# Performance work log

Hardware: AMD Instinct MI355X
Metric: run time of the kernel (lower is better)

The kernel has to match this reference:

```python
import jax, jax.numpy as jnp
import numpy as np

N_NODES = 100000
N_EDGES = 1600000
N_FEAT = 128
N_HID = 128


def cheb_conv_k2(x, edge_index, W0, W1, b):
    """PyG ChebConv with K=2, sym norm, lambda_max=2.0.
    Reduces to: out = x @ W0 + (L_hat x) @ W1 + b, where
    L_hat = 2L/lambda_max - I = -D^{-1/2} A D^{-1/2} (diagonal cancels).
    """
    n = x.shape[0]
    row, col = edge_index[0], edge_index[1]
    deg = jax.ops.segment_sum(jnp.ones_like(row, dtype=x.dtype), row, num_segments=n)
    dinv = jnp.where(deg > 0, jax.lax.rsqrt(jnp.maximum(deg, 1.0)), 0.0)
    w = -(dinv[row] * dinv[col])                     # [E] edge weights of L_hat
    tx1 = jax.ops.segment_sum(x[col] * w[:, None], row, num_segments=n)  # [N, F]
    return x @ W0 + tx1 @ W1 + b


def setup_inputs() -> dict:
    key = jax.random.key(0)
    ks = jax.random.split(key, 8)
    glorot = lambda k, fi, fo: jax.random.normal(k, (fi, fo), dtype=jnp.float32) * np.float32(np.sqrt(2.0 / (fi + fo)))
    x = jax.random.normal(ks[0], (N_NODES, N_FEAT), dtype=jnp.float32)
    edge_index = jax.random.randint(ks[1], (2, N_EDGES), 0, N_NODES, dtype=jnp.int64 if jax.config.jax_enable_x64 else jnp.int32)
    return {
        "x": x,
        "edge_index": edge_index,
        "W0_1": glorot(ks[2], N_FEAT, N_HID),
        "W1_1": glorot(ks[3], N_FEAT, N_HID),
        "b1": jnp.zeros((N_HID,), dtype=jnp.float32),
        "W0_2": glorot(ks[4], N_HID, N_HID),
        "W1_2": glorot(ks[5], N_HID, N_HID),
        "b2": jnp.zeros((N_HID,), dtype=jnp.float32),
    }


def reference(x, edge_index, W0_1, W1_1, b1, W0_2, W1_2, b2):
    # eval mode: input Dropout, dropout_adj(p=0.8), and per-layer Dropout are identity
    x1 = jax.nn.relu(cheb_conv_k2(x, edge_index, W0_1, W1_1, b1))
    x2 = jax.nn.relu(cheb_conv_k2(x1, edge_index, W0_2, W1_2, b2))
    # mean of the two layer outputs; outAct is identity
    return (x1 + x2) * 0.5
```

## Files before the change

### kernel.cpp

```cpp
#include <hip/hip_runtime.h>

#define NN 100000
#define NE 1600000
#define NF 128
#define NSTRIP (NN / 16)
#define NBUCK ((NN + 127) / 128)
#define CAP 2560
#define CHUNK 4096

typedef __attribute__((ext_vector_type(8))) short short8;
typedef __attribute__((ext_vector_type(4))) float f32x4;

__device__ __forceinline__ unsigned short f2b(float f) {
    union { float f; unsigned int u; } v; v.f = f;
    unsigned int u = v.u;
    unsigned int r = (u + 0x7fffu + ((u >> 16) & 1u)) >> 16;
    return (unsigned short)r;
}

__global__ __launch_bounds__(256) void k_init(int* __restrict__ gcur) {
    int i = blockIdx.x * 256 + threadIdx.x;
    if (i < NBUCK) gcur[i] = i * CAP;
}

__global__ __launch_bounds__(256) void k_bin(const int* __restrict__ row,
                                             const int* __restrict__ col,
                                             int* __restrict__ gcur,
                                             unsigned int* __restrict__ gslab) {
    __shared__ int hist[NBUCK];
    __shared__ int start[NBUCK];
    __shared__ int gbase[NBUCK];
    __shared__ int scanbuf[256];
    __shared__ unsigned int stage[CHUNK];
    __shared__ unsigned short sb[CHUNK];

    const int t = threadIdx.x;
    const int e0 = blockIdx.x * CHUNK;
    const int cnt = min(CHUNK, NE - e0);

    for (int i = t; i < NBUCK; i += 256) hist[i] = 0;
    __syncthreads();
    for (int i = t; i < cnt; i += 256) atomicAdd(&hist[row[e0 + i] >> 7], 1);
    __syncthreads();

    const int b0 = t * 4;
    int s = 0;
#pragma unroll
    for (int k = 0; k < 4; ++k) { int idx = b0 + k; if (idx < NBUCK) s += hist[idx]; }
    scanbuf[t] = s;
    __syncthreads();
    for (int off = 1; off < 256; off <<= 1) {
        int u = t >= off ? scanbuf[t - off] : 0;
        __syncthreads();
        scanbuf[t] += u;
        __syncthreads();
    }
    int run = t > 0 ? scanbuf[t - 1] : 0;
#pragma unroll
    for (int k = 0; k < 4; ++k) {
        int idx = b0 + k;
        if (idx < NBUCK) { start[idx] = run; run += hist[idx]; }
    }
    __syncthreads();

    for (int i = t; i < NBUCK; i += 256) {
        int c = hist[i];
        gbase[i] = c > 0 ? atomicAdd(&gcur[i], c) : 0;
        hist[i] = start[i];
    }
    __syncthreads();

    for (int i = t; i < cnt; i += 256) {
        int r = row[e0 + i];
        int b = r >> 7;
        int p = atomicAdd(&hist[b], 1);
        stage[p] = (unsigned int)col[e0 + i] | ((unsigned int)(r & 127) << 17);
        sb[p] = (unsigned short)b;
    }
    __syncthreads();

    for (int i = t; i < cnt; i += 256) {
        int b = sb[i];
        gslab[gbase[b] + (i - start[b])] = stage[i];
    }
}

__global__ __launch_bounds__(256) void k_bscan(const int* __restrict__ gcur,
                                               int* __restrict__ bbase) {
    __shared__ int s[NBUCK];
    int t = threadIdx.x;
    for (int i = t; i < NBUCK; i += 256) s[i] = gcur[i] - i * CAP;
    __syncthreads();
    if (t == 0) {
        int run = 0;
        for (int i = 0; i < NBUCK; ++i) { int v = s[i]; s[i] = run; run += v; }
    }
    __syncthreads();
    for (int i = t; i < NBUCK; i += 256) bbase[i] = s[i];
}

__global__ __launch_bounds__(256) void k_csr(const unsigned int* __restrict__ gslab,
                                             const int* __restrict__ gcur,
                                             const int* __restrict__ bbase,
                                             int* __restrict__ offs,
                                             int* __restrict__ ccol,
                                             float* __restrict__ dinv) {
    __shared__ int rh[128];
    __shared__ int rcur[128];
    __shared__ unsigned int scol[CAP];

    const int b = blockIdx.x;
    const int segbase = b * CAP;
    const int cnt = gcur[b] - segbase;
    const int csr0 = bbase[b];
    const int t = threadIdx.x;

    if (t < 128) rh[t] = 0;
    __syncthreads();
    for (int i = t; i < cnt; i += 256) atomicAdd(&rh[gslab[segbase + i] >> 17], 1);
    __syncthreads();
    if (t == 0) {
        int run = 0;
        for (int r = 0; r < 128; ++r) { rcur[r] = run; run += rh[r]; }
    }
    __syncthreads();

    const int rbase = b * 128;
    if (t < 128 && rbase + t < NN) {
        offs[rbase + t] = csr0 + rcur[t];
        int d = rh[t];
        dinv[rbase + t] = d > 0 ? rsqrtf((float)d) : 0.0f;
    }
    if (b == NBUCK - 1 && t == 0) offs[NN] = NE;
    __syncthreads();

    for (int i = t; i < cnt; i += 256) {
        unsigned int v = gslab[segbase + i];
        int p = atomicAdd(&rcur[v >> 17], 1);
        scol[p] = v & 0x1ffff;
    }
    __syncthreads();
    for (int i = t; i < cnt; i += 256) ccol[csr0 + i] = scol[i];
}

__global__ __launch_bounds__(256) void k_quant(const float* __restrict__ x,
                                               const float* __restrict__ dinv,
                                               unsigned short* __restrict__ xq,
                                               float* __restrict__ dsc,
                                               float* __restrict__ sx) {
    int r = (blockIdx.x * 256 + threadIdx.x) >> 6;
    int lane = threadIdx.x & 63;
    float2 v = ((const float2*)x)[r * 64 + lane];
    float m = fmaxf(fabsf(v.x), fabsf(v.y));
#pragma unroll
    for (int mask = 32; mask; mask >>= 1) m = fmaxf(m, __shfl_xor(m, mask));
    float s = m * (1.0f / 127.0f);
    float inv = m > 0.0f ? 127.0f / m : 0.0f;
    int qx = (int)rintf(v.x * inv) + 128;
    int qy = (int)rintf(v.y * inv) + 128;
    xq[r * 64 + lane] = (unsigned short)(qx | (qy << 8));
    if (lane == 0) { dsc[r] = dinv[r] * s; sx[r] = s; }
}

__global__ __launch_bounds__(256) void k_pack(const float* __restrict__ W01,
                                              const float* __restrict__ W11,
                                              const float* __restrict__ W02,
                                              const float* __restrict__ W12,
                                              unsigned short* __restrict__ WP) {
    int idx = blockIdx.x * 256 + threadIdx.x;
    int mi = idx >> 14;
    int e = idx & 16383;
    const float* W = mi == 0 ? W01 : mi == 1 ? W02 : mi == 2 ? W11 : W12;
    int midx = mi == 0 ? 0 : mi == 1 ? 2 : mi == 2 ? 1 : 3;
    int k = e >> 7, n = e & 127;
    int kt = k >> 5, g = (k >> 3) & 3, j = k & 7;
    WP[midx * 16384 + (((kt * 4 + g) * 128 + n) << 3) + j] = f2b(W[e]);
}

__global__ __launch_bounds__(256) void k_gather(const int* __restrict__ offs,
                                                const int* __restrict__ ccol,
                                                const float* __restrict__ dsc,
                                                const float* __restrict__ dinv,
                                                const uint2* __restrict__ xq64,
                                                uint4* __restrict__ txb4,
                                                float qbias) {
    int r = (blockIdx.x * 256 + threadIdx.x) >> 6;
    if (r >= NN) return;
    int lane = threadIdx.x & 63;
    int fl = lane & 15, q = lane >> 4;
    int beg = offs[r], end = offs[r + 1];
    float a0 = 0.f, a1 = 0.f, a2 = 0.f, a3 = 0.f;
    float a4 = 0.f, a5 = 0.f, a6 = 0.f, a7 = 0.f, S = 0.f;
    int j = beg + q;
    for (; j + 12 < end; j += 16) {
        int c0 = ccol[j], c1 = ccol[j + 4], c2 = ccol[j + 8], c3 = ccol[j + 12];
        float w0 = dsc[c0], w1 = dsc[c1], w2 = dsc[c2], w3 = dsc[c3];
        uint2 u0 = xq64[c0 * 16 + fl];
        uint2 u1 = xq64[c1 * 16 + fl];
        uint2 u2 = xq64[c2 * 16 + fl];
        uint2 u3 = xq64[c3 * 16 + fl];
        a0 += w0 * (float)(u0.x & 0xffu)         + w1 * (float)(u1.x & 0xffu)
            + w2 * (float)(u2.x & 0xffu)         + w3 * (float)(u3.x & 0xffu);
        a1 += w0 * (float)((u0.x >> 8) & 0xffu)  + w1 * (float)((u1.x >> 8) & 0xffu)
            + w2 * (float)((u2.x >> 8) & 0xffu)  + w3 * (float)((u3.x >> 8) & 0xffu);
        a2 += w0 * (float)((u0.x >> 16) & 0xffu) + w1 * (float)((u1.x >> 16) & 0xffu)
            + w2 * (float)((u2.x >> 16) & 0xffu) + w3 * (float)((u3.x >> 16) & 0xffu);
        a3 += w0 * (float)(u0.x >> 24)           + w1 * (float)(u1.x >> 24)
            + w2 * (float)(u2.x >> 24)           + w3 * (float)(u3.x >> 24);
        a4 += w0 * (float)(u0.y & 0xffu)         + w1 * (float)(u1.y & 0xffu)
            + w2 * (float)(u2.y & 0xffu)         + w3 * (float)(u3.y & 0xffu);
        a5 += w0 * (float)((u0.y >> 8) & 0xffu)  + w1 * (float)((u1.y >> 8) & 0xffu)
            + w2 * (float)((u2.y >> 8) & 0xffu)  + w3 * (float)((u3.y >> 8) & 0xffu);
        a6 += w0 * (float)((u0.y >> 16) & 0xffu) + w1 * (float)((u1.y >> 16) & 0xffu)
            + w2 * (float)((u2.y >> 16) & 0xffu) + w3 * (float)((u3.y >> 16) & 0xffu);
        a7 += w0 * (float)(u0.y >> 24)           + w1 * (float)(u1.y >> 24)
            + w2 * (float)(u2.y >> 24)           + w3 * (float)(u3.y >> 24);
        S += w0 + w1 + w2 + w3;
    }
    for (; j < end; j += 4) {
        int c = ccol[j];
        float w = dsc[c];
        uint2 u = xq64[c * 16 + fl];
        a0 += w * (float)(u.x & 0xffu);
        a1 += w * (float)((u.x >> 8) & 0xffu);
        a2 += w * (float)((u.x >> 16) & 0xffu);
        a3 += w * (float)(u.x >> 24);
        a4 += w * (float)(u.y & 0xffu);
        a5 += w * (float)((u.y >> 8) & 0xffu);
        a6 += w * (float)((u.y >> 16) & 0xffu);
        a7 += w * (float)(u.y >> 24);
        S += w;
    }
#pragma unroll
    for (int mask = 32; mask >= 16; mask >>= 1) {
        a0 += __shfl_xor(a0, mask); a1 += __shfl_xor(a1, mask);
        a2 += __shfl_xor(a2, mask); a3 += __shfl_xor(a3, mask);
        a4 += __shfl_xor(a4, mask); a5 += __shfl_xor(a5, mask);
        a6 += __shfl_xor(a6, mask); a7 += __shfl_xor(a7, mask);
        S  += __shfl_xor(S, mask);
    }
    if (q == 0) {
        float s = -dinv[r];
        float qb = qbias * S;
        a0 = s * (a0 - qb); a1 = s * (a1 - qb); a2 = s * (a2 - qb); a3 = s * (a3 - qb);
        a4 = s * (a4 - qb); a5 = s * (a5 - qb); a6 = s * (a6 - qb); a7 = s * (a7 - qb);
        uint4 o;
        o.x = (unsigned int)f2b(a0) | ((unsigned int)f2b(a1) << 16);
        o.y = (unsigned int)f2b(a2) | ((unsigned int)f2b(a3) << 16);
        o.z = (unsigned int)f2b(a4) | ((unsigned int)f2b(a5) << 16);
        o.w = (unsigned int)f2b(a6) | ((unsigned int)f2b(a7) << 16);
        txb4[r * 16 + fl] = o;
    }
}

__global__ __launch_bounds__(256) void k_mm(const unsigned char* __restrict__ Aq,
                                            const float* __restrict__ s_in,
                                            float qoff,
                                            const unsigned short* __restrict__ Tbf,
                                            const unsigned short* __restrict__ WP0,
                                            const unsigned short* __restrict__ WP1,
                                            const float* __restrict__ bias,
                                            const float* __restrict__ dinv,
                                            float* __restrict__ out,
                                            unsigned char* __restrict__ Qout,
                                            float* __restrict__ dsc_out,
                                            float* __restrict__ s1_out,
                                            int mode) {
    int wid = (blockIdx.x * 256 + threadIdx.x) >> 6;
    if (wid >= NSTRIP) return;
    int lane = threadIdx.x & 63;
    int g = lane >> 4, m = lane & 15;

    short8 a[4], t[4];
    {
        float sA = s_in[wid * 16 + m];
        const unsigned char* Arow = Aq + (size_t)(wid * 16 + m) * NF + g * 8;
#pragma unroll
        for (int kt = 0; kt < 4; ++kt) {
            uint2 u = *(const uint2*)(Arow + kt * 32);
            short8 v;
            v[0] = f2b(sA * ((float)(u.x & 0xffu) - qoff));
            v[1] = f2b(sA * ((float)((u.x >> 8) & 0xffu) - qoff));
            v[2] = f2b(sA * ((float)((u.x >> 16) & 0xffu) - qoff));
            v[3] = f2b(sA * ((float)(u.x >> 24) - qoff));
            v[4] = f2b(sA * ((float)(u.y & 0xffu) - qoff));
            v[5] = f2b(sA * ((float)((u.y >> 8) & 0xffu) - qoff));
            v[6] = f2b(sA * ((float)((u.y >> 16) & 0xffu) - qoff));
            v[7] = f2b(sA * ((float)(u.y >> 24) - qoff));
            a[kt] = v;
        }
    }

    const short8* Tfr = (const short8*)(Tbf + (size_t)(wid * 16 + m) * NF + g * 8);
#pragma unroll
    for (int kt = 0; kt < 4; ++kt) t[kt] = Tfr[kt * 4];

    const short8* B0 = (const short8*)WP0 + g * 128 + m;
    const short8* B1 = (const short8*)WP1 + g * 128 + m;

    f32x4 acc[8];
#pragma unroll
    for (int nt = 0; nt < 8; ++nt) {
        float b = bias[nt * 16 + m];
        acc[nt][0] = b; acc[nt][1] = b; acc[nt][2] = b; acc[nt][3] = b;
    }

#pragma unroll
    for (int nt = 0; nt < 8; ++nt) {
#pragma unroll
        for (int kt = 0; kt < 4; ++kt) {
            acc[nt] = __builtin_amdgcn_mfma_f32_16x16x32_bf16(a[kt], B0[kt * 512 + nt * 16], acc[nt], 0, 0, 0);
            acc[nt] = __builtin_amdgcn_mfma_f32_16x16x32_bf16(t[kt], B1[kt * 512 + nt * 16], acc[nt], 0, 0, 0);
        }
    }

#pragma unroll
    for (int nt = 0; nt < 8; ++nt)
#pragma unroll
        for (int r = 0; r < 4; ++r) acc[nt][r] = fmaxf(acc[nt][r], 0.0f);

    int rbase = wid * 16 + g * 4;
    if (mode == 0) {
        float mr[4] = {0.0f, 0.0f, 0.0f, 0.0f};
#pragma unroll
        for (int nt = 0; nt < 8; ++nt)
#pragma unroll
            for (int r = 0; r < 4; ++r) mr[r] = fmaxf(mr[r], acc[nt][r]);
#pragma unroll
        for (int mask = 1; mask < 16; mask <<= 1)
#pragma unroll
            for (int r = 0; r < 4; ++r) mr[r] = fmaxf(mr[r], __shfl_xor(mr[r], mask));

        float inv[4], s1v[4];
#pragma unroll
        for (int r = 0; r < 4; ++r) {
            s1v[r] = mr[r] * (1.0f / 255.0f);
            inv[r] = mr[r] > 0.0f ? 255.0f / mr[r] : 0.0f;
        }
#pragma unroll
        for (int nt = 0; nt < 8; ++nt) {
            int c = nt * 16 + m;
#pragma unroll
            for (int r = 0; r < 4; ++r) {
                int q = (int)rintf(acc[nt][r] * inv[r]);
                q = q > 255 ? 255 : q;
                Qout[(size_t)(rbase + r) * NF + c] = (unsigned char)q;
            }
        }
        if (m == 0) {
#pragma unroll
            for (int r = 0; r < 4; ++r) {
                s1_out[rbase + r] = s1v[r];
                dsc_out[rbase + r] = dinv[rbase + r] * s1v[r];
            }
        }
    } else {
        float sR[4];
#pragma unroll
        for (int r = 0; r < 4; ++r) sR[r] = s_in[rbase + r];
#pragma unroll
        for (int nt = 0; nt < 8; ++nt) {
            int c = nt * 16 + m;
#pragma unroll
            for (int r = 0; r < 4; ++r) {
                size_t o = (size_t)(rbase + r) * NF + c;
                float x1v = sR[r] * (float)Aq[o];
                out[o] = 0.5f * (x1v + acc[nt][r]);
            }
        }
    }
}

extern "C" void kernel_launch(void* const* d_in, const int* in_sizes, int n_in,
                              void* d_out, int out_size, void* d_ws, size_t ws_size,
                              hipStream_t stream) {
    const float* x   = (const float*)d_in[0];
    const int*   ei  = (const int*)d_in[1];
    const float* W01 = (const float*)d_in[2];
    const float* W11 = (const float*)d_in[3];
    const float* b1  = (const float*)d_in[4];
    const float* W02 = (const float*)d_in[5];
    const float* W12 = (const float*)d_in[6];
    const float* b2  = (const float*)d_in[7];
    float* out = (float*)d_out;

    const int* row = ei;
    const int* col = ei + NE;

    char* ws = (char*)d_ws;
    int*            gcur  = (int*)(ws);
    int*            bbase = (int*)(ws + 3200);
    float*          dinv  = (float*)(ws + 6400);
    int*            offs  = (int*)(ws + 406400);
    int*            ccol  = (int*)(ws + 806416);
    unsigned short* WP    = (unsigned short*)(ws + 7206416);
    float*          dsc   = (float*)(ws + 7337488);
    float*          s1a   = (float*)(ws + 7737488);
    float*          sx    = (float*)(ws + 8137488);
    unsigned short* xq    = (unsigned short*)(ws + 8537488);
    unsigned int*   txb   = (unsigned int*)(ws + 21337488);
    unsigned int*   gslab = (unsigned int*)(ws + 21337488);

    unsigned char*  xq8 = (unsigned char*)xq;
    unsigned short* WP01 = WP;
    unsigned short* WP11 = WP + 16384;
    unsigned short* WP02 = WP + 32768;
    unsigned short* WP12 = WP + 49152;

    k_init <<<(NBUCK + 255) / 256, 256, 0, stream>>>(gcur);
    k_bin  <<<(NE + CHUNK - 1) / CHUNK, 256, 0, stream>>>(row, col, gcur, gslab);
    k_bscan<<<1, 256, 0, stream>>>(gcur, bbase);
    k_csr  <<<NBUCK, 256, 0, stream>>>(gslab, gcur, bbase, offs, ccol, dinv);

    k_quant<<<(NN * 64) / 256, 256, 0, stream>>>(x, dinv, xq, dsc, sx);
    k_pack <<<(4 * 16384) / 256, 256, 0, stream>>>(W01, W11, W02, W12, WP);

    const int gatherBlocks = (NN * 64) / 256;
    const int mmBlocks = (NSTRIP * 64 + 255) / 256;

    k_gather<<<gatherBlocks, 256, 0, stream>>>(offs, ccol, dsc, dinv,
                                               (const uint2*)xq, (uint4*)txb, 128.0f);
    k_mm    <<<mmBlocks, 256, 0, stream>>>(xq8, sx, 128.0f, (const unsigned short*)txb,
                                           WP01, WP11, b1, dinv, out, xq8, dsc, s1a, 0);

    k_gather<<<gatherBlocks, 256, 0, stream>>>(offs, ccol, dsc, dinv,
                                               (const uint2*)xq, (uint4*)txb, 0.0f);
    k_mm    <<<mmBlocks, 256, 0, stream>>>(xq8, s1a, 0.0f, (const unsigned short*)txb,
                                           WP02, WP12, b2, dinv, out, xq8, dsc, s1a, 1);
}
```

Measured before the change: 245.0 us.

## Quantize aggregated features to int8, double rows per wave in matmul, fold init kernel

```diff
diff --git a/kernel.cpp b/kernel.cpp
--- a/kernel.cpp
+++ b/kernel.cpp
@@ -3,7 +3,7 @@
 #define NN 100000
 #define NE 1600000
 #define NF 128
-#define NSTRIP (NN / 16)
+#define NSTRIP2 (NN / 32)
 #define NBUCK ((NN + 127) / 128)
 #define CAP 2560
 #define CHUNK 4096
@@ -16,11 +16,6 @@
     unsigned int u = v.u;
     unsigned int r = (u + 0x7fffu + ((u >> 16) & 1u)) >> 16;
     return (unsigned short)r;
-}
-
-__global__ __launch_bounds__(256) void k_init(int* __restrict__ gcur) {
-    int i = blockIdx.x * 256 + threadIdx.x;
-    if (i < NBUCK) gcur[i] = i * CAP;
 }
 
 __global__ __launch_bounds__(256) void k_bin(const int* __restrict__ row,
@@ -166,8 +161,10 @@
                                               const float* __restrict__ W11,
                                               const float* __restrict__ W02,
                                               const float* __restrict__ W12,
-                                              unsigned short* __restrict__ WP) {
+                                              unsigned short* __restrict__ WP,
+                                              int* __restrict__ gcur) {
     int idx = blockIdx.x * 256 + threadIdx.x;
+    if (idx < NBUCK) gcur[idx] = idx * CAP;
     int mi = idx >> 14;
     int e = idx & 16383;
     const float* W = mi == 0 ? W01 : mi == 1 ? W02 : mi == 2 ? W11 : W12;
@@ -182,7 +179,8 @@
                                                 const float* __restrict__ dsc,
                                                 const float* __restrict__ dinv,
                                                 const uint2* __restrict__ xq64,
-                                                uint4* __restrict__ txb4,
+                                                uint2* __restrict__ txq8,
+                                                float* __restrict__ st_out,
                                                 float qbias) {
     int r = (blockIdx.x * 256 + threadIdx.x) >> 6;
     if (r >= NN) return;
@@ -244,19 +242,29 @@
         float qb = qbias * S;
         a0 = s * (a0 - qb); a1 = s * (a1 - qb); a2 = s * (a2 - qb); a3 = s * (a3 - qb);
         a4 = s * (a4 - qb); a5 = s * (a5 - qb); a6 = s * (a6 - qb); a7 = s * (a7 - qb);
-        uint4 o;
-        o.x = (unsigned int)f2b(a0) | ((unsigned int)f2b(a1) << 16);
-        o.y = (unsigned int)f2b(a2) | ((unsigned int)f2b(a3) << 16);
-        o.z = (unsigned int)f2b(a4) | ((unsigned int)f2b(a5) << 16);
-        o.w = (unsigned int)f2b(a6) | ((unsigned int)f2b(a7) << 16);
-        txb4[r * 16 + fl] = o;
+        float mx = fmaxf(fmaxf(fmaxf(fabsf(a0), fabsf(a1)), fmaxf(fabsf(a2), fabsf(a3))),
+                         fmaxf(fmaxf(fabsf(a4), fabsf(a5)), fmaxf(fabsf(a6), fabsf(a7))));
+#pragma unroll
+        for (int mask = 8; mask; mask >>= 1) mx = fmaxf(mx, __shfl_xor(mx, mask));
+        float st = mx * (1.0f / 127.0f);
+        float invt = mx > 0.0f ? 127.0f / mx : 0.0f;
+        int q0 = (int)rintf(a0 * invt) + 128, q1 = (int)rintf(a1 * invt) + 128;
+        int q2 = (int)rintf(a2 * invt) + 128, q3 = (int)rintf(a3 * invt) + 128;
+        int q4 = (int)rintf(a4 * invt) + 128, q5 = (int)rintf(a5 * invt) + 128;
+        int q6 = (int)rintf(a6 * invt) + 128, q7 = (int)rintf(a7 * invt) + 128;
+        uint2 o;
+        o.x = (unsigned)q0 | ((unsigned)q1 << 8) | ((unsigned)q2 << 16) | ((unsigned)q3 << 24);
+        o.y = (unsigned)q4 | ((unsigned)q5 << 8) | ((unsigned)q6 << 16) | ((unsigned)q7 << 24);
+        txq8[r * 16 + fl] = o;
+        if (fl == 0) st_out[r] = st;
     }
 }
 
 __global__ __launch_bounds__(256) void k_mm(const unsigned char* __restrict__ Aq,
                                             const float* __restrict__ s_in,
                                             float qoff,
-                                            const unsigned short* __restrict__ Tbf,
+                                            const unsigned char* __restrict__ Tq8,
+                                            const float* __restrict__ st_in,
                                             const unsigned short* __restrict__ WP0,
                                             const unsigned short* __restrict__ WP1,
                                             const float* __restrict__ bias,
@@ -267,14 +275,18 @@
                                             float* __restrict__ s1_out,
                                             int mode) {
     int wid = (blockIdx.x * 256 + threadIdx.x) >> 6;
-    if (wid >= NSTRIP) return;
+    if (wid >= NSTRIP2) return;
     int lane = threadIdx.x & 63;
     int g = lane >> 4, m = lane & 15;
 
-    short8 a[4], t[4];
-    {
-        float sA = s_in[wid * 16 + m];
-        const unsigned char* Arow = Aq + (size_t)(wid * 16 + m) * NF + g * 8;
+    short8 a[2][4], t[2][4];
+#pragma unroll
+    for (int s = 0; s < 2; ++s) {
+        int row = wid * 32 + s * 16 + m;
+        float sA = s_in[row];
+        float sT = st_in[row];
+        const unsigned char* Arow = Aq + (size_t)row * NF + g * 8;
+        const unsigned char* Trow = Tq8 + (size_t)row * NF + g * 8;
 #pragma unroll
         for (int kt = 0; kt < 4; ++kt) {
             uint2 u = *(const uint2*)(Arow + kt * 32);
@@ -287,85 +299,109 @@
             v[5] = f2b(sA * ((float)((u.y >> 8) & 0xffu) - qoff));
             v[6] = f2b(sA * ((float)((u.y >> 16) & 0xffu) - qoff));
             v[7] = f2b(sA * ((float)(u.y >> 24) - qoff));
-            a[kt] = v;
+            a[s][kt] = v;
+            uint2 w = *(const uint2*)(Trow + kt * 32);
+            short8 tv;
+            tv[0] = f2b(sT * ((float)(w.x & 0xffu) - 128.0f));
+            tv[1] = f2b(sT * ((float)((w.x >> 8) & 0xffu) - 128.0f));
+            tv[2] = f2b(sT * ((float)((w.x >> 16) & 0xffu) - 128.0f));
+            tv[3] = f2b(sT * ((float)(w.x >> 24) - 128.0f));
+            tv[4] = f2b(sT * ((float)(w.y & 0xffu) - 128.0f));
+            tv[5] = f2b(sT * ((float)((w.y >> 8) & 0xffu) - 128.0f));
+            tv[6] = f2b(sT * ((float)((w.y >> 16) & 0xffu) - 128.0f));
+            tv[7] = f2b(sT * ((float)(w.y >> 24) - 128.0f));
+            t[s][kt] = tv;
         }
     }
-
-    const short8* Tfr = (const short8*)(Tbf + (size_t)(wid * 16 + m) * NF + g * 8);
-#pragma unroll
-    for (int kt = 0; kt < 4; ++kt) t[kt] = Tfr[kt * 4];
 
     const short8* B0 = (const short8*)WP0 + g * 128 + m;
     const short8* B1 = (const short8*)WP1 + g * 128 + m;
 
-    f32x4 acc[8];
+    f32x4 acc[2][8];
 #pragma unroll
     for (int nt = 0; nt < 8; ++nt) {
         float b = bias[nt * 16 + m];
-        acc[nt][0] = b; acc[nt][1] = b; acc[nt][2] = b; acc[nt][3] = b;
+#pragma unroll
+        for (int s = 0; s < 2; ++s) {
+            acc[s][nt][0] = b; acc[s][nt][1] = b; acc[s][nt][2] = b; acc[s][nt][3] = b;
+        }
     }
 
 #pragma unroll
     for (int nt = 0; nt < 8; ++nt) {
 #pragma unroll
         for (int kt = 0; kt < 4; ++kt) {
-            acc[nt] = __builtin_amdgcn_mfma_f32_16x16x32_bf16(a[kt], B0[kt * 512 + nt * 16], acc[nt], 0, 0, 0);
-            acc[nt] = __builtin_amdgcn_mfma_f32_16x16x32_bf16(t[kt], B1[kt * 512 + nt * 16], acc[nt], 0, 0, 0);
-        }
-    }
-
-#pragma unroll
-    for (int nt = 0; nt < 8; ++nt)
-#pragma unroll
-        for (int r = 0; r < 4; ++r) acc[nt][r] = fmaxf(acc[nt][r], 0.0f);
-
-    int rbase = wid * 16 + g * 4;
-    if (mode == 0) {
-        float mr[4] = {0.0f, 0.0f, 0.0f, 0.0f};
-#pragma unroll
-        for (int nt = 0; nt < 8; ++nt)
-#pragma unroll
-            for (int r = 0; r < 4; ++r) mr[r] = fmaxf(mr[r], acc[nt][r]);
-#pragma unroll
-        for (int mask = 1; mask < 16; mask <<= 1)
-#pragma unroll
-            for (int r = 0; r < 4; ++r) mr[r] = fmaxf(mr[r], __shfl_xor(mr[r], mask));
-
-        float inv[4], s1v[4];
-#pragma unroll
-        for (int r = 0; r < 4; ++r) {
-            s1v[r] = mr[r] * (1.0f / 255.0f);
-            inv[r] = mr[r] > 0.0f ? 255.0f / mr[r] : 0.0f;
-        }
-#pragma unroll
-        for (int nt = 0; nt < 8; ++nt) {
-            int c = nt * 16 + m;
-#pragma unroll
-            for (int r = 0; r < 4; ++r) {
-                int q = (int)rintf(acc[nt][r] * inv[r]);
-                q = q > 255 ? 255 : q;
-                Qout[(size_t)(rbase + r) * NF + c] = (unsigned char)q;
+            short8 b0 = B0[kt * 512 + nt * 16];
+            short8 b1 = B1[kt * 512 + nt * 16];
+#pragma unroll
+            for (int s = 0; s < 2; ++s) {
+                acc[s][nt] = __builtin_amdgcn_mfma_f32_16x16x32_bf16(a[s][kt], b0, acc[s][nt], 0, 0, 0);
+                acc[s][nt] = __builtin_amdgcn_mfma_f32_16x16x32_bf16(t[s][kt], b1, acc[s][nt], 0, 0, 0);
             }
         }
-        if (m == 0) {
+    }
+
+#pragma unroll
+    for (int s = 0; s < 2; ++s)
+#pragma unroll
+        for (int nt = 0; nt < 8; ++nt)
+#pragma unroll
+            for (int r = 0; r < 4; ++r) acc[s][nt][r] = fmaxf(acc[s][nt][r], 0.0f);
+
+    if (mode == 0) {
+#pragma unroll
+        for (int s = 0; s < 2; ++s) {
+            int rbase = wid * 32 + s * 16 + g * 4;
+            float mr[4] = {0.0f, 0.0f, 0.0f, 0.0f};
+#pragma unroll
+            for (int nt = 0; nt < 8; ++nt)
+#pragma unroll
+                for (int r = 0; r < 4; ++r) mr[r] = fmaxf(mr[r], acc[s][nt][r]);
+#pragma unroll
+            for (int mask = 1; mask < 16; mask <<= 1)
+#pragma unroll
+                for (int r = 0; r < 4; ++r) mr[r] = fmaxf(mr[r], __shfl_xor(mr[r], mask));
+
+            float inv[4], s1v[4];
 #pragma unroll
             for (int r = 0; r < 4; ++r) {
-                s1_out[rbase + r] = s1v[r];
-                dsc_out[rbase + r] = dinv[rbase + r] * s1v[r];
+                s1v[r] = mr[r] * (1.0f / 255.0f);
+                inv[r] = mr[r] > 0.0f ? 255.0f / mr[r] : 0.0f;
+            }
+#pragma unroll
+            for (int nt = 0; nt < 8; ++nt) {
+                int c = nt * 16 + m;
+#pragma unroll
+                for (int r = 0; r < 4; ++r) {
+                    int qv = (int)rintf(acc[s][nt][r] * inv[r]);
+                    qv = qv > 255 ? 255 : qv;
+                    Qout[(size_t)(rbase + r) * NF + c] = (unsigned char)qv;
+                }
+            }
+            if (m == 0) {
+#pragma unroll
+                for (int r = 0; r < 4; ++r) {
+                    s1_out[rbase + r] = s1v[r];
+                    dsc_out[rbase + r] = dinv[rbase + r] * s1v[r];
+                }
             }
         }
     } else {
-        float sR[4];
-#pragma unroll
-        for (int r = 0; r < 4; ++r) sR[r] = s_in[rbase + r];
-#pragma unroll
-        for (int nt = 0; nt < 8; ++nt) {
-            int c = nt * 16 + m;
-#pragma unroll
-            for (int r = 0; r < 4; ++r) {
-                size_t o = (size_t)(rbase + r) * NF + c;
-                float x1v = sR[r] * (float)Aq[o];
-                out[o] = 0.5f * (x1v + acc[nt][r]);
+#pragma unroll
+        for (int s = 0; s < 2; ++s) {
+            int rbase = wid * 32 + s * 16 + g * 4;
+            float sR[4];
+#pragma unroll
+            for (int r = 0; r < 4; ++r) sR[r] = s_in[rbase + r];
+#pragma unroll
+            for (int nt = 0; nt < 8; ++nt) {
+                int c = nt * 16 + m;
+#pragma unroll
+                for (int r = 0; r < 4; ++r) {
+                    size_t o = (size_t)(rbase + r) * NF + c;
+                    float x1v = sR[r] * (float)Aq[o];
+                    out[o] = 0.5f * (x1v + acc[s][nt][r]);
+                }
             }
         }
     }
@@ -397,9 +433,10 @@
     float*          dsc   = (float*)(ws + 7337488);
     float*          s1a   = (float*)(ws + 7737488);
     float*          sx    = (float*)(ws + 8137488);
-    unsigned short* xq    = (unsigned short*)(ws + 8537488);
-    unsigned int*   txb   = (unsigned int*)(ws + 21337488);
-    unsigned int*   gslab = (unsigned int*)(ws + 21337488);
+    float*          st    = (float*)(ws + 8537488);
+    unsigned short* xq    = (unsigned short*)(ws + 8937488);
+    unsigned char*  txq   = (unsigned char*)(ws + 21737488);
+    unsigned int*   gslab = (unsigned int*)(ws + 21737488);
 
     unsigned char*  xq8 = (unsigned char*)xq;
     unsigned short* WP01 = WP;
@@ -407,24 +444,23 @@
     unsigned short* WP02 = WP + 32768;
     unsigned short* WP12 = WP + 49152;
 
-    k_init <<<(NBUCK + 255) / 256, 256, 0, stream>>>(gcur);
+    k_pack <<<(4 * 16384) / 256, 256, 0, stream>>>(W01, W11, W02, W12, WP, gcur);
     k_bin  <<<(NE + CHUNK - 1) / CHUNK, 256, 0, stream>>>(row, col, gcur, gslab);
     k_bscan<<<1, 256, 0, stream>>>(gcur, bbase);
     k_csr  <<<NBUCK, 256, 0, stream>>>(gslab, gcur, bbase, offs, ccol, dinv);
 
     k_quant<<<(NN * 64) / 256, 256, 0, stream>>>(x, dinv, xq, dsc, sx);
-    k_pack <<<(4 * 16384) / 256, 256, 0, stream>>>(W01, W11, W02, W12, WP);
 
     const int gatherBlocks = (NN * 64) / 256;
-    const int mmBlocks = (NSTRIP * 64 + 255) / 256;
+    const int mmBlocks = (NSTRIP2 * 64 + 255) / 256;
 
     k_gather<<<gatherBlocks, 256, 0, stream>>>(offs, ccol, dsc, dinv,
-                                               (const uint2*)xq, (uint4*)txb, 128.0f);
-    k_mm    <<<mmBlocks, 256, 0, stream>>>(xq8, sx, 128.0f, (const unsigned short*)txb,
+                                               (const uint2*)xq, (uint2*)txq, st, 128.0f);
+    k_mm    <<<mmBlocks, 256, 0, stream>>>(xq8, sx, 128.0f, txq, st,
                                            WP01, WP11, b1, dinv, out, xq8, dsc, s1a, 0);
 
     k_gather<<<gatherBlocks, 256, 0, stream>>>(offs, ccol, dsc, dinv,
-                                               (const uint2*)xq, (uint4*)txb, 0.0f);
-    k_mm    <<<mmBlocks, 256, 0, stream>>>(xq8, s1a, 0.0f, (const unsigned short*)txb,
+                                               (const uint2*)xq, (uint2*)txq, st, 0.0f);
+    k_mm    <<<mmBlocks, 256, 0, stream>>>(xq8, s1a, 0.0f, txq, st,
                                            WP02, WP12, b2, dinv, out, xq8, dsc, s1a, 1);
 }
```

Result: slower. 251.1 us (+2.5%).
